# Performance work log

Measured on AMD Instinct MI355X. Metric: run time of the kernel, lower is better.

The kernel has to match this reference:

```python
import jax, jax.numpy as jnp
import numpy as np

N_NODES = 100000
N_EDGES = 1250000
F_RAW = 48      # raw node feature dim
F_LOC = 16      # location embedding dim
F1 = 48         # filters_1
F_OUT = 64      # out_channels


def _glorot(key, shape):
    fan_in, fan_out = shape[0], shape[1]
    scale = jnp.sqrt(6.0 / (fan_in + fan_out)).astype(jnp.float32)
    return jax.random.uniform(key, shape, jnp.float32, -1.0, 1.0) * scale


def setup_inputs() -> dict:
    key = jax.random.key(0)
    k_e, k_x, k_l, k_w1, k_w2 = jax.random.split(key, 5)
    edge_indices = jax.random.randint(k_e, (2, N_EDGES), 0, N_NODES, dtype=jnp.int64)
    features = jax.random.normal(k_x, (N_NODES, F_RAW), jnp.float32)
    location_embedding = jax.random.normal(k_l, (N_NODES, F_LOC), jnp.float32)
    W1 = _glorot(k_w1, (F_RAW + F_LOC, F1))
    b1 = jnp.zeros((F1,), jnp.float32)
    W2 = _glorot(k_w2, (F1 + F_LOC, F_OUT))
    b2 = jnp.zeros((F_OUT,), jnp.float32)
    return {"edge_indices": edge_indices, "features": features,
            "location_embedding": location_embedding,
            "W1": W1, "b1": b1, "W2": W2, "b2": b2}


def gcn_conv(x, src, dst, W, b, n_nodes):
    """PyG GCNConv: add self-loops, symmetric normalization, linear + bias."""
    h = x @ W  # [N, F_out]
    # degree counts include the self-loop (+1)
    deg = jnp.zeros((n_nodes,), h.dtype).at[dst].add(1.0) + 1.0
    dinv = jax.lax.rsqrt(deg)  # deg >= 1 so always finite
    coef = dinv[src] * dinv[dst]  # [E]
    agg = jnp.zeros((n_nodes, h.shape[1]), h.dtype).at[dst].add(h[src] * coef[:, None])
    # self-loop contribution: dinv[i]^2 * h[i]
    return agg + h * (dinv * dinv)[:, None] + b


def reference(edge_indices, features, location_embedding, W1, b1, W2, b2):
    src, dst = edge_indices[0], edge_indices[1]
    n = features.shape[0]
    x = jnp.concatenate([features, location_embedding], axis=-1)
    x = gcn_conv(x, src, dst, W1, b1, n)
    x = jax.nn.relu(x)
    # dropout is identity in eval mode (reference is inference semantics)
    x = jnp.concatenate([x, location_embedding], axis=-1)
    x = gcn_conv(x, src, dst, W2, b2, n)
    return x
```

## Files before the change

kernel.cpp:

```cpp
#include <hip/hip_runtime.h>
#include <hip/hip_fp16.h>

#define N_NODES 100000
#define N_EDGES 1250000
#define F_RAW 48
#define F_LOC 16
#define F1 48
#define F_OUT 64

#define NBUK 391
#define PADB 4096
#define NB2 500
#define CH2 (N_EDGES / NB2)

typedef _Float16 half8_t __attribute__((ext_vector_type(8)));
typedef float floatx4 __attribute__((ext_vector_type(4)));

__device__ void wprep_dev(const float* W, __half* Wpk, int M, int CT) {
    int lane = threadIdx.x;
    if (lane >= 64) return;
    for (int ct = 0; ct < CT; ++ct)
        for (int kt = 0; kt < 2; ++kt)
            for (int j = 0; j < 8; ++j) {
                int k = kt * 32 + (lane >> 4) * 8 + j;
                int c = ct * 16 + (lane & 15);
                Wpk[((ct * 2 + kt) * 64 + lane) * 8 + j] =
                    __float2half(W[k * M + c]);
            }
}

__device__ __forceinline__ void load_edge(const void* edges, int is32, int e,
                                          int& s, int& d) {
    if (is32) {
        const int* p = (const int*)edges;
        s = p[e];
        d = p[N_EDGES + e];
    } else {
        const long long* p = (const long long*)edges;
        s = (int)p[e];
        d = (int)p[N_EDGES + e];
    }
}

__global__ __launch_bounds__(512) void k_prep2(const void* edges,
                                               const float* W1, __half* wpk1,
                                               const float* W2, __half* wpk2,
                                               int* __restrict__ cursor,
                                               unsigned* __restrict__ binned) {
    int b = blockIdx.x, t = threadIdx.x;
    if (b >= NB2) {
        if (b == NB2)
            wprep_dev(W1, wpk1, F1, 3);
        else
            wprep_dev(W2, wpk2, F_OUT, 4);
        return;
    }
    __shared__ int hist[NBUK];
    __shared__ int2 stash[CH2];
    __shared__ int s_any;
    if (t == 0) s_any = 0;
    for (int k = t; k < NBUK; k += 512) hist[k] = 0;
    __syncthreads();
    int e0 = b * CH2;
    const unsigned* eu = (const unsigned*)edges;
    if (eu[2 * (e0 + t) + 1] != 0u) atomicOr(&s_any, 1);
    __syncthreads();
    int is32 = s_any;
    for (int i = t; i < CH2; i += 512) {
        int s, d;
        load_edge(edges, is32, e0 + i, s, d);
        int bk = d >> 8;
        stash[i] = make_int2(bk, ((d & 255) << 17) | s);
        atomicAdd(&hist[bk], 1);
    }
    __syncthreads();
    for (int k = t; k < NBUK; k += 512) {
        int c = hist[k];
        hist[k] = (c ? atomicAdd(&cursor[k], c) : 0) + k * PADB;
    }
    __syncthreads();
    for (int i = t; i < CH2; i += 512) {
        int2 sd = stash[i];
        int p = atomicAdd(&hist[sd.x], 1);
        binned[p] = (unsigned)sd.y;
    }
}

__global__ __launch_bounds__(256) void k_bucket(
    const unsigned* __restrict__ binned, const int* __restrict__ cursor,
    float* __restrict__ dinv, int2* __restrict__ rowse,
    unsigned* __restrict__ csr4) {
    int k = blockIdx.x, t = threadIdx.x;
    int lane = t & 63, wv = t >> 6;
    __shared__ int ldeg[256];
    __shared__ int wcnt[256];
    __shared__ int ws4[4];
    int base = k * PADB;
    int len = cursor[k];
    ldeg[t] = 0;
    __syncthreads();
    for (int i = t; i < len; i += 256)
        atomicAdd(&ldeg[binned[base + i] >> 17], 1);
    __syncthreads();
    int degv = ldeg[t];
    int x = degv;
#pragma unroll
    for (int off = 1; off < 64; off <<= 1) {
        int u = __shfl_up(x, off);
        if (lane >= off) x += u;
    }
    if (lane == 63) ws4[wv] = x;
    __syncthreads();
    int woff = 0;
    for (int w = 0; w < wv; ++w) woff += ws4[w];
    int excl = woff + x - degv;
    int node = k * 256 + t;
    if (node < N_NODES) {
        dinv[node] = rsqrtf((float)degv + 1.0f);
        rowse[node] = make_int2(base + excl, base + excl + degv);
    }
    wcnt[t] = base + excl;
    __syncthreads();
    for (int i = t; i < len; i += 256) {
        unsigned ent = binned[base + i];
        int p = atomicAdd(&wcnt[ent >> 17], 1);
        csr4[p] = ent & 0x1FFFFu;
    }
}

__global__ __launch_bounds__(256) void k_coef(unsigned* __restrict__ csr4,
                                              const float* __restrict__ dinv,
                                              const int* __restrict__ cursor) {
    int k = blockIdx.x;
    int end = k * PADB + cursor[k];
    for (int i = k * PADB + threadIdx.x; i < end; i += 256) {
        unsigned s = csr4[i];
        csr4[i] = (s << 14) | (unsigned)__half_as_ushort(__float2half(dinv[s]));
    }
}

__global__ __launch_bounds__(256) void k_gemm1(const float* __restrict__ feat,
                                               const float* __restrict__ loc,
                                               const __half* __restrict__ Wpk,
                                               __half* __restrict__ Y) {
    int wid = threadIdx.x >> 6;
    int lane = threadIdx.x & 63;
    int nb = (blockIdx.x * 4 + wid) * 32;
    if (nb >= N_NODES) return;
    half8_t b[3][2];
#pragma unroll
    for (int ct = 0; ct < 3; ++ct)
#pragma unroll
        for (int kt = 0; kt < 2; ++kt)
            b[ct][kt] = *reinterpret_cast<const half8_t*>(
                Wpk + ((ct * 2 + kt) * 64 + lane) * 8);
    int r = lane & 15;
    int slot = lane >> 4;
    half8_t a[2][2];
#pragma unroll
    for (int rt = 0; rt < 2; ++rt)
#pragma unroll
        for (int kt = 0; kt < 2; ++kt) {
            int sl = kt * 4 + slot;
            int node = nb + rt * 16 + r;
            const float* sp = (sl < 6)
                                  ? feat + (size_t)node * F_RAW + sl * 8
                                  : loc + (size_t)node * F_LOC + (sl - 6) * 8;
            float4 f0 = reinterpret_cast<const float4*>(sp)[0];
            float4 f1 = reinterpret_cast<const float4*>(sp)[1];
            half8_t h;
            h[0] = (_Float16)f0.x;
            h[1] = (_Float16)f0.y;
            h[2] = (_Float16)f0.z;
            h[3] = (_Float16)f0.w;
            h[4] = (_Float16)f1.x;
            h[5] = (_Float16)f1.y;
            h[6] = (_Float16)f1.z;
            h[7] = (_Float16)f1.w;
            a[rt][kt] = h;
        }
    floatx4 acc[2][3];
#pragma unroll
    for (int rt = 0; rt < 2; ++rt)
#pragma unroll
        for (int ct = 0; ct < 3; ++ct) {
            floatx4 z = {0.f, 0.f, 0.f, 0.f};
            z = __builtin_amdgcn_mfma_f32_16x16x32_f16(a[rt][0], b[ct][0], z, 0, 0, 0);
            z = __builtin_amdgcn_mfma_f32_16x16x32_f16(a[rt][1], b[ct][1], z, 0, 0, 0);
            acc[rt][ct] = z;
        }
    int row0 = (lane >> 4) * 4;
    int col = lane & 15;
#pragma unroll
    for (int rt = 0; rt < 2; ++rt)
#pragma unroll
        for (int ct = 0; ct < 3; ++ct)
#pragma unroll
            for (int j = 0; j < 4; ++j) {
                int node = nb + rt * 16 + row0 + j;
                Y[(size_t)node * 64 + ct * 16 + col] = __float2half(acc[rt][ct][j]);
            }
    int node = nb + (lane & 31);
    int slotp = 6 + (lane >> 5);
    *reinterpret_cast<int4*>(Y + (size_t)node * 64 + slotp * 8) =
        make_int4(0, 0, 0, 0);
}

__global__ __launch_bounds__(256) void k_gemm2(const __half* __restrict__ X,
                                               const __half* __restrict__ Wpk,
                                               __half* __restrict__ Y) {
    int wid = threadIdx.x >> 6;
    int lane = threadIdx.x & 63;
    int nb = (blockIdx.x * 4 + wid) * 32;
    if (nb >= N_NODES) return;
    half8_t b[4][2];
#pragma unroll
    for (int ct = 0; ct < 4; ++ct)
#pragma unroll
        for (int kt = 0; kt < 2; ++kt)
            b[ct][kt] = *reinterpret_cast<const half8_t*>(
                Wpk + ((ct * 2 + kt) * 64 + lane) * 8);
    int r = lane & 15;
    int ks = (lane >> 4) * 8;
    half8_t a[2][2];
#pragma unroll
    for (int rt = 0; rt < 2; ++rt)
#pragma unroll
        for (int kt = 0; kt < 2; ++kt)
            a[rt][kt] = *reinterpret_cast<const half8_t*>(
                X + ((size_t)(nb + rt * 16 + r) * 64 + kt * 32 + ks));
    floatx4 acc[2][4];
#pragma unroll
    for (int rt = 0; rt < 2; ++rt)
#pragma unroll
        for (int ct = 0; ct < 4; ++ct) {
            floatx4 z = {0.f, 0.f, 0.f, 0.f};
            z = __builtin_amdgcn_mfma_f32_16x16x32_f16(a[rt][0], b[ct][0], z, 0, 0, 0);
            z = __builtin_amdgcn_mfma_f32_16x16x32_f16(a[rt][1], b[ct][1], z, 0, 0, 0);
            acc[rt][ct] = z;
        }
    int row0 = (lane >> 4) * 4;
    int col = lane & 15;
#pragma unroll
    for (int rt = 0; rt < 2; ++rt)
#pragma unroll
        for (int ct = 0; ct < 4; ++ct)
#pragma unroll
            for (int j = 0; j < 4; ++j) {
                int node = nb + rt * 16 + row0 + j;
                Y[(size_t)node * 64 + ct * 16 + col] = __float2half(acc[rt][ct][j]);
            }
}

__device__ __forceinline__ __half2 c2_from(unsigned A) {
    unsigned b = A & 0x3FFFu;
    unsigned p = b | (b << 16);
    return *reinterpret_cast<__half2*>(&p);
}

__device__ __forceinline__ void fma8h(const int4& p, __half2 c2, __half2 a[4]) {
    const __half2* h = reinterpret_cast<const __half2*>(&p);
#pragma unroll
    for (int j = 0; j < 4; ++j) a[j] = __hfma2(h[j], c2, a[j]);
}

__device__ __forceinline__ __half2 shfl_xor_h2(__half2 v, int m) {
    int i = *reinterpret_cast<int*>(&v);
    i = __shfl_xor(i, m);
    return *reinterpret_cast<__half2*>(&i);
}

__global__ __launch_bounds__(256) void k_agg1(
    const __half* __restrict__ h1h, const float* __restrict__ dinv,
    const int2* __restrict__ rowse, const unsigned* __restrict__ csr4,
    const float* __restrict__ loc, const float* __restrict__ b1,
    __half* __restrict__ x1h) {
    int wave = threadIdx.x >> 6;
    int lane = threadIdx.x & 63;
    int grp = lane >> 3;
    int l8 = lane & 7;
    int node = blockIdx.x * 4 + wave;
    if (node >= N_NODES) return;
    int2 se = rowse[node];
    int r0 = se.x, r1 = se.y;
    const char* h1l = reinterpret_cast<const char*>(h1h) + (l8 << 4);
    float di = dinv[node];
    int4 hs = *reinterpret_cast<const int4*>(h1l + ((size_t)node << 7));
    int len = r1 - r0;
    int L = (len + 7) >> 3;
    int gs = r0 + grp * L;
    int ge = gs + L;
    if (ge > r1) ge = r1;
    __half2 z2 = __float2half2_rn(0.f);
    __half2 a0[4] = {z2, z2, z2, z2};
    __half2 a1[4] = {z2, z2, z2, z2};
    int e = gs;
    for (; e + 1 < ge; e += 2) {
        unsigned A = csr4[e];
        unsigned B = csr4[e + 1];
        int4 vA = *reinterpret_cast<const int4*>(h1l + ((A >> 14) << 7));
        int4 vB = *reinterpret_cast<const int4*>(h1l + ((B >> 14) << 7));
        fma8h(vA, c2_from(A), a0);
        fma8h(vB, c2_from(B), a1);
    }
    if (e < ge) {
        unsigned A = csr4[e];
        int4 vA = *reinterpret_cast<const int4*>(h1l + ((A >> 14) << 7));
        fma8h(vA, c2_from(A), a0);
    }
#pragma unroll
    for (int j = 0; j < 4; ++j) a0[j] = __hadd2(a0[j], a1[j]);
#pragma unroll
    for (int j = 0; j < 4; ++j) {
        a0[j] = __hadd2(a0[j], shfl_xor_h2(a0[j], 8));
        a0[j] = __hadd2(a0[j], shfl_xor_h2(a0[j], 16));
        a0[j] = __hadd2(a0[j], shfl_xor_h2(a0[j], 32));
    }
    if (lane < 8) {
        __half2 q[4];
        if (l8 < 6) {
            float d2 = di * di;
            const float4* b1v = reinterpret_cast<const float4*>(b1);
            float4 bA = b1v[l8 * 2];
            float4 bB = b1v[l8 * 2 + 1];
            float bb[8] = {bA.x, bA.y, bA.z, bA.w, bB.x, bB.y, bB.z, bB.w};
            const __half2* hh = reinterpret_cast<const __half2*>(&hs);
            float o[8];
#pragma unroll
            for (int j = 0; j < 4; ++j) {
                float2 t = __half22float2(hh[j]);
                float2 ag = __half22float2(a0[j]);
                o[2 * j] = fmaxf(fmaf(ag.x, di, fmaf(t.x, d2, bb[2 * j])), 0.f);
                o[2 * j + 1] =
                    fmaxf(fmaf(ag.y, di, fmaf(t.y, d2, bb[2 * j + 1])), 0.f);
            }
#pragma unroll
            for (int j = 0; j < 4; ++j)
                q[j] = __halves2half2(__float2half(o[2 * j]),
                                      __float2half(o[2 * j + 1]));
        } else {
            const float* lp = loc + (size_t)node * F_LOC + (l8 - 6) * 8;
            float4 f0 = reinterpret_cast<const float4*>(lp)[0];
            float4 f1 = reinterpret_cast<const float4*>(lp)[1];
            q[0] = __halves2half2(__float2half(f0.x), __float2half(f0.y));
            q[1] = __halves2half2(__float2half(f0.z), __float2half(f0.w));
            q[2] = __halves2half2(__float2half(f1.x), __float2half(f1.y));
            q[3] = __halves2half2(__float2half(f1.z), __float2half(f1.w));
        }
        reinterpret_cast<int4*>(x1h)[(size_t)node * 8 + l8] =
            *reinterpret_cast<int4*>(q);
    }
}

__global__ __launch_bounds__(256) void k_out(
    const __half* __restrict__ h2h, const float* __restrict__ dinv,
    const int2* __restrict__ rowse, const unsigned* __restrict__ csr4,
    const float* __restrict__ b2, float* __restrict__ out) {
    int wave = threadIdx.x >> 6;
    int lane = threadIdx.x & 63;
    int grp = lane >> 3;
    int l8 = lane & 7;
    int node = blockIdx.x * 4 + wave;
    if (node >= N_NODES) return;
    int2 se = rowse[node];
    int r0 = se.x, r1 = se.y;
    const char* h2l = reinterpret_cast<const char*>(h2h) + (l8 << 4);
    float di = dinv[node];
    int4 hs = *reinterpret_cast<const int4*>(h2l + ((size_t)node << 7));
    int len = r1 - r0;
    int L = (len + 7) >> 3;
    int gs = r0 + grp * L;
    int ge = gs + L;
    if (ge > r1) ge = r1;
    __half2 z2 = __float2half2_rn(0.f);
    __half2 a0[4] = {z2, z2, z2, z2};
    __half2 a1[4] = {z2, z2, z2, z2};
    int e = gs;
    for (; e + 1 < ge; e += 2) {
        unsigned A = csr4[e];
        unsigned B = csr4[e + 1];
        int4 vA = *reinterpret_cast<const int4*>(h2l + ((A >> 14) << 7));
        int4 vB = *reinterpret_cast<const int4*>(h2l + ((B >> 14) << 7));
        fma8h(vA, c2_from(A), a0);
        fma8h(vB, c2_from(B), a1);
    }
    if (e < ge) {
        unsigned A = csr4[e];
        int4 vA = *reinterpret_cast<const int4*>(h2l + ((A >> 14) << 7));
        fma8h(vA, c2_from(A), a0);
    }
#pragma unroll
    for (int j = 0; j < 4; ++j) a0[j] = __hadd2(a0[j], a1[j]);
#pragma unroll
    for (int j = 0; j < 4; ++j) {
        a0[j] = __hadd2(a0[j], shfl_xor_h2(a0[j], 8));
        a0[j] = __hadd2(a0[j], shfl_xor_h2(a0[j], 16));
        a0[j] = __hadd2(a0[j], shfl_xor_h2(a0[j], 32));
    }
    if (lane < 8) {
        float d2 = di * di;
        const float4* b2v = reinterpret_cast<const float4*>(b2);
        float4 bA = b2v[l8 * 2];
        float4 bB = b2v[l8 * 2 + 1];
        float bb[8] = {bA.x, bA.y, bA.z, bA.w, bB.x, bB.y, bB.z, bB.w};
        const __half2* hh = reinterpret_cast<const __half2*>(&hs);
        float o[8];
#pragma unroll
        for (int j = 0; j < 4; ++j) {
            float2 t = __half22float2(hh[j]);
            float2 ag = __half22float2(a0[j]);
            o[2 * j] = fmaf(ag.x, di, fmaf(t.x, d2, bb[2 * j]));
            o[2 * j + 1] = fmaf(ag.y, di, fmaf(t.y, d2, bb[2 * j + 1]));
        }
        float4* ov = reinterpret_cast<float4*>(out + (size_t)node * F_OUT);
        ov[l8 * 2] = make_float4(o[0], o[1], o[2], o[3]);
        ov[l8 * 2 + 1] = make_float4(o[4], o[5], o[6], o[7]);
    }
}

extern "C" void kernel_launch(void* const* d_in, const int* in_sizes, int n_in,
                              void* d_out, int out_size, void* d_ws,
                              size_t ws_size, hipStream_t stream) {
    const void* edges = d_in[0];
    const float* feat = (const float*)d_in[1];
    const float* loc = (const float*)d_in[2];
    const float* W1 = (const float*)d_in[3];
    const float* b1 = (const float*)d_in[4];
    const float* W2 = (const float*)d_in[5];
    const float* b2 = (const float*)d_in[6];
    float* out = (float*)d_out;

    char* ws = (char*)d_ws;
    float* dinv = (float*)(ws + 0);
    int2* rowse = (int2*)(ws + 400000);
    int* cursor = (int*)(ws + 1200000);
    unsigned* binned = (unsigned*)(ws + 1201664);
    unsigned* csr4 = (unsigned*)(ws + 7607808);
    __half* h1h = (__half*)(ws + 14013952);
    __half* x1h = (__half*)(ws + 26813952);
    __half* h2h = (__half*)(ws + 39613952);
    __half* wpk1 = (__half*)(ws + 52413952);
    __half* wpk2 = (__half*)(ws + 52420096);

    hipMemsetAsync(cursor, 0, NBUK * 4, stream);

    k_prep2<<<NB2 + 2, 512, 0, stream>>>(edges, W1, wpk1, W2, wpk2, cursor,
                                         binned);
    k_bucket<<<NBUK, 256, 0, stream>>>(binned, cursor, dinv, rowse, csr4);
    k_coef<<<NBUK, 256, 0, stream>>>(csr4, dinv, cursor);

    int gblocks = (N_NODES / 32 + 3) / 4;
    k_gemm1<<<gblocks, 256, 0, stream>>>(feat, loc, wpk1, h1h);
    k_agg1<<<(N_NODES + 3) / 4, 256, 0, stream>>>(h1h, dinv, rowse, csr4, loc,
                                                  b1, x1h);
    k_gemm2<<<gblocks, 256, 0, stream>>>(x1h, wpk2, h2h);
    k_out<<<(N_NODES + 3) / 4, 256, 0, stream>>>(h2h, dinv, rowse, csr4, b2,
                                                 out);
}
```

Before: 149.9 us.

## Fuse coef with gemm1 and fuse layer-1 aggregation with gemm2 via LDS

Merges the coefficient-packing kernel and the first GEMM into one launch, with block ranges split by blockIdx. Fuses the layer-1 aggregation with the second GEMM: each 512-thread block aggregates 32 nodes into an LDS tile, then runs MFMA on it to produce h2 directly. This removes the x1h global round-trip and two kernel launches. In exchange, each block now does both the gather-bound aggregation and the GEMM, and every wave waits at the sync for the slowest node in its tile.

```diff
diff --git a/kernel.cpp b/kernel.cpp
--- a/kernel.cpp
+++ b/kernel.cpp
@@ -12,6 +12,9 @@
 #define PADB 4096
 #define NB2 500
 #define CH2 (N_EDGES / NB2)
+
+#define GB1 ((N_NODES / 32 + 3) / 4)
+#define LROW 144
 
 typedef _Float16 half8_t __attribute__((ext_vector_type(8)));
 typedef float floatx4 __attribute__((ext_vector_type(4)));
@@ -128,24 +131,24 @@
     }
 }
 
-__global__ __launch_bounds__(256) void k_coef(unsigned* __restrict__ csr4,
-                                              const float* __restrict__ dinv,
-                                              const int* __restrict__ cursor) {
-    int k = blockIdx.x;
-    int end = k * PADB + cursor[k];
-    for (int i = k * PADB + threadIdx.x; i < end; i += 256) {
-        unsigned s = csr4[i];
-        csr4[i] = (s << 14) | (unsigned)__half_as_ushort(__float2half(dinv[s]));
-    }
-}
-
-__global__ __launch_bounds__(256) void k_gemm1(const float* __restrict__ feat,
-                                               const float* __restrict__ loc,
-                                               const __half* __restrict__ Wpk,
-                                               __half* __restrict__ Y) {
+__global__ __launch_bounds__(256) void k_cg1(
+    unsigned* __restrict__ csr4, const float* __restrict__ dinv,
+    const int* __restrict__ cursor, const float* __restrict__ feat,
+    const float* __restrict__ loc, const __half* __restrict__ Wpk,
+    __half* __restrict__ Y) {
+    if (blockIdx.x < NBUK) {
+        int k = blockIdx.x;
+        int end = k * PADB + cursor[k];
+        for (int i = k * PADB + threadIdx.x; i < end; i += 256) {
+            unsigned s = csr4[i];
+            csr4[i] =
+                (s << 14) | (unsigned)__half_as_ushort(__float2half(dinv[s]));
+        }
+        return;
+    }
     int wid = threadIdx.x >> 6;
     int lane = threadIdx.x & 63;
-    int nb = (blockIdx.x * 4 + wid) * 32;
+    int nb = ((blockIdx.x - NBUK) * 4 + wid) * 32;
     if (nb >= N_NODES) return;
     half8_t b[3][2];
 #pragma unroll
@@ -206,52 +209,6 @@
         make_int4(0, 0, 0, 0);
 }
 
-__global__ __launch_bounds__(256) void k_gemm2(const __half* __restrict__ X,
-                                               const __half* __restrict__ Wpk,
-                                               __half* __restrict__ Y) {
-    int wid = threadIdx.x >> 6;
-    int lane = threadIdx.x & 63;
-    int nb = (blockIdx.x * 4 + wid) * 32;
-    if (nb >= N_NODES) return;
-    half8_t b[4][2];
-#pragma unroll
-    for (int ct = 0; ct < 4; ++ct)
-#pragma unroll
-        for (int kt = 0; kt < 2; ++kt)
-            b[ct][kt] = *reinterpret_cast<const half8_t*>(
-                Wpk + ((ct * 2 + kt) * 64 + lane) * 8);
-    int r = lane & 15;
-    int ks = (lane >> 4) * 8;
-    half8_t a[2][2];
-#pragma unroll
-    for (int rt = 0; rt < 2; ++rt)
-#pragma unroll
-        for (int kt = 0; kt < 2; ++kt)
-            a[rt][kt] = *reinterpret_cast<const half8_t*>(
-                X + ((size_t)(nb + rt * 16 + r) * 64 + kt * 32 + ks));
-    floatx4 acc[2][4];
-#pragma unroll
-    for (int rt = 0; rt < 2; ++rt)
-#pragma unroll
-        for (int ct = 0; ct < 4; ++ct) {
-            floatx4 z = {0.f, 0.f, 0.f, 0.f};
-            z = __builtin_amdgcn_mfma_f32_16x16x32_f16(a[rt][0], b[ct][0], z, 0, 0, 0);
-            z = __builtin_amdgcn_mfma_f32_16x16x32_f16(a[rt][1], b[ct][1], z, 0, 0, 0);
-            acc[rt][ct] = z;
-        }
-    int row0 = (lane >> 4) * 4;
-    int col = lane & 15;
-#pragma unroll
-    for (int rt = 0; rt < 2; ++rt)
-#pragma unroll
-        for (int ct = 0; ct < 4; ++ct)
-#pragma unroll
-            for (int j = 0; j < 4; ++j) {
-                int node = nb + rt * 16 + row0 + j;
-                Y[(size_t)node * 64 + ct * 16 + col] = __float2half(acc[rt][ct][j]);
-            }
-}
-
 __device__ __forceinline__ __half2 c2_from(unsigned A) {
     unsigned b = A & 0x3FFFu;
     unsigned p = b | (b << 16);
@@ -270,85 +227,113 @@
     return *reinterpret_cast<__half2*>(&i);
 }
 
-__global__ __launch_bounds__(256) void k_agg1(
+__global__ __launch_bounds__(512) void k_aggemm(
     const __half* __restrict__ h1h, const float* __restrict__ dinv,
     const int2* __restrict__ rowse, const unsigned* __restrict__ csr4,
     const float* __restrict__ loc, const float* __restrict__ b1,
-    __half* __restrict__ x1h) {
-    int wave = threadIdx.x >> 6;
-    int lane = threadIdx.x & 63;
+    const __half* __restrict__ Wpk2, __half* __restrict__ h2h) {
+    __shared__ __align__(16) char lds_x1[32 * LROW];
+    int t = threadIdx.x;
+    int w = t >> 6;
+    int lane = t & 63;
     int grp = lane >> 3;
     int l8 = lane & 7;
-    int node = blockIdx.x * 4 + wave;
-    if (node >= N_NODES) return;
-    int2 se = rowse[node];
-    int r0 = se.x, r1 = se.y;
+    int nb = blockIdx.x * 32;
     const char* h1l = reinterpret_cast<const char*>(h1h) + (l8 << 4);
-    float di = dinv[node];
-    int4 hs = *reinterpret_cast<const int4*>(h1l + ((size_t)node << 7));
-    int len = r1 - r0;
-    int L = (len + 7) >> 3;
-    int gs = r0 + grp * L;
-    int ge = gs + L;
-    if (ge > r1) ge = r1;
-    __half2 z2 = __float2half2_rn(0.f);
-    __half2 a0[4] = {z2, z2, z2, z2};
-    __half2 a1[4] = {z2, z2, z2, z2};
-    int e = gs;
-    for (; e + 1 < ge; e += 2) {
-        unsigned A = csr4[e];
-        unsigned B = csr4[e + 1];
-        int4 vA = *reinterpret_cast<const int4*>(h1l + ((A >> 14) << 7));
-        int4 vB = *reinterpret_cast<const int4*>(h1l + ((B >> 14) << 7));
-        fma8h(vA, c2_from(A), a0);
-        fma8h(vB, c2_from(B), a1);
-    }
-    if (e < ge) {
-        unsigned A = csr4[e];
-        int4 vA = *reinterpret_cast<const int4*>(h1l + ((A >> 14) << 7));
-        fma8h(vA, c2_from(A), a0);
-    }
-#pragma unroll
-    for (int j = 0; j < 4; ++j) a0[j] = __hadd2(a0[j], a1[j]);
+#pragma unroll
+    for (int it = 0; it < 4; ++it) {
+        int nl = w * 4 + it;
+        int node = nb + nl;
+        int2 se = rowse[node];
+        int r0 = se.x, r1 = se.y;
+        float di = dinv[node];
+        int4 hs = *reinterpret_cast<const int4*>(h1l + ((size_t)node << 7));
+        int len = r1 - r0;
+        int L = (len + 7) >> 3;
+        int gs = r0 + grp * L;
+        int ge = gs + L;
+        if (ge > r1) ge = r1;
+        __half2 z2 = __float2half2_rn(0.f);
+        __half2 a0[4] = {z2, z2, z2, z2};
+        __half2 a1[4] = {z2, z2, z2, z2};
+        int e = gs;
+        for (; e + 1 < ge; e += 2) {
+            unsigned A = csr4[e];
+            unsigned B = csr4[e + 1];
+            int4 vA = *reinterpret_cast<const int4*>(h1l + ((A >> 14) << 7));
+            int4 vB = *reinterpret_cast<const int4*>(h1l + ((B >> 14) << 7));
+            fma8h(vA, c2_from(A), a0);
+            fma8h(vB, c2_from(B), a1);
+        }
+        if (e < ge) {
+            unsigned A = csr4[e];
+            int4 vA = *reinterpret_cast<const int4*>(h1l + ((A >> 14) << 7));
+            fma8h(vA, c2_from(A), a0);
+        }
+#pragma unroll
+        for (int j = 0; j < 4; ++j) a0[j] = __hadd2(a0[j], a1[j]);
+#pragma unroll
+        for (int j = 0; j < 4; ++j) {
+            a0[j] = __hadd2(a0[j], shfl_xor_h2(a0[j], 8));
+            a0[j] = __hadd2(a0[j], shfl_xor_h2(a0[j], 16));
+            a0[j] = __hadd2(a0[j], shfl_xor_h2(a0[j], 32));
+        }
+        if (lane < 8) {
+            __half2 q[4];
+            if (l8 < 6) {
+                float d2 = di * di;
+                const float4* b1v = reinterpret_cast<const float4*>(b1);
+                float4 bA = b1v[l8 * 2];
+                float4 bB = b1v[l8 * 2 + 1];
+                float bb[8] = {bA.x, bA.y, bA.z, bA.w, bB.x, bB.y, bB.z, bB.w};
+                const __half2* hh = reinterpret_cast<const __half2*>(&hs);
+#pragma unroll
+                for (int j = 0; j < 4; ++j) {
+                    float2 tt = __half22float2(hh[j]);
+                    float2 ag = __half22float2(a0[j]);
+                    float o0 =
+                        fmaxf(fmaf(ag.x, di, fmaf(tt.x, d2, bb[2 * j])), 0.f);
+                    float o1 = fmaxf(
+                        fmaf(ag.y, di, fmaf(tt.y, d2, bb[2 * j + 1])), 0.f);
+                    q[j] = __halves2half2(__float2half(o0), __float2half(o1));
+                }
+            } else {
+                const float* lp = loc + (size_t)node * F_LOC + (l8 - 6) * 8;
+                float4 f0 = reinterpret_cast<const float4*>(lp)[0];
+                float4 f1 = reinterpret_cast<const float4*>(lp)[1];
+                q[0] = __halves2half2(__float2half(f0.x), __float2half(f0.y));
+                q[1] = __halves2half2(__float2half(f0.z), __float2half(f0.w));
+                q[2] = __halves2half2(__float2half(f1.x), __float2half(f1.y));
+                q[3] = __halves2half2(__float2half(f1.z), __float2half(f1.w));
+            }
+            *reinterpret_cast<int4*>(&lds_x1[nl * LROW + l8 * 16]) =
+                *reinterpret_cast<int4*>(q);
+        }
+    }
+    __syncthreads();
+    int rt = w >> 2;
+    int ct = w & 3;
+    half8_t bfr[2];
+#pragma unroll
+    for (int kt = 0; kt < 2; ++kt)
+        bfr[kt] = *reinterpret_cast<const half8_t*>(
+            Wpk2 + ((ct * 2 + kt) * 64 + lane) * 8);
+    int r = lane & 15;
+    int ks = (lane >> 4) * 8;
+    half8_t afr[2];
+#pragma unroll
+    for (int kt = 0; kt < 2; ++kt)
+        afr[kt] = *reinterpret_cast<const half8_t*>(
+            &lds_x1[(rt * 16 + r) * LROW + kt * 64 + ks * 2]);
+    floatx4 z = {0.f, 0.f, 0.f, 0.f};
+    z = __builtin_amdgcn_mfma_f32_16x16x32_f16(afr[0], bfr[0], z, 0, 0, 0);
+    z = __builtin_amdgcn_mfma_f32_16x16x32_f16(afr[1], bfr[1], z, 0, 0, 0);
+    int row0 = (lane >> 4) * 4;
+    int col = lane & 15;
 #pragma unroll
     for (int j = 0; j < 4; ++j) {
-        a0[j] = __hadd2(a0[j], shfl_xor_h2(a0[j], 8));
-        a0[j] = __hadd2(a0[j], shfl_xor_h2(a0[j], 16));
-        a0[j] = __hadd2(a0[j], shfl_xor_h2(a0[j], 32));
-    }
-    if (lane < 8) {
-        __half2 q[4];
-        if (l8 < 6) {
-            float d2 = di * di;
-            const float4* b1v = reinterpret_cast<const float4*>(b1);
-            float4 bA = b1v[l8 * 2];
-            float4 bB = b1v[l8 * 2 + 1];
-            float bb[8] = {bA.x, bA.y, bA.z, bA.w, bB.x, bB.y, bB.z, bB.w};
-            const __half2* hh = reinterpret_cast<const __half2*>(&hs);
-            float o[8];
-#pragma unroll
-            for (int j = 0; j < 4; ++j) {
-                float2 t = __half22float2(hh[j]);
-                float2 ag = __half22float2(a0[j]);
-                o[2 * j] = fmaxf(fmaf(ag.x, di, fmaf(t.x, d2, bb[2 * j])), 0.f);
-                o[2 * j + 1] =
-                    fmaxf(fmaf(ag.y, di, fmaf(t.y, d2, bb[2 * j + 1])), 0.f);
-            }
-#pragma unroll
-            for (int j = 0; j < 4; ++j)
-                q[j] = __halves2half2(__float2half(o[2 * j]),
-                                      __float2half(o[2 * j + 1]));
-        } else {
-            const float* lp = loc + (size_t)node * F_LOC + (l8 - 6) * 8;
-            float4 f0 = reinterpret_cast<const float4*>(lp)[0];
-            float4 f1 = reinterpret_cast<const float4*>(lp)[1];
-            q[0] = __halves2half2(__float2half(f0.x), __float2half(f0.y));
-            q[1] = __halves2half2(__float2half(f0.z), __float2half(f0.w));
-            q[2] = __halves2half2(__float2half(f1.x), __float2half(f1.y));
-            q[3] = __halves2half2(__float2half(f1.z), __float2half(f1.w));
-        }
-        reinterpret_cast<int4*>(x1h)[(size_t)node * 8 + l8] =
-            *reinterpret_cast<int4*>(q);
+        int node = nb + rt * 16 + row0 + j;
+        h2h[(size_t)node * 64 + ct * 16 + col] = __float2half(z[j]);
     }
 }
 
@@ -437,23 +422,22 @@
     unsigned* binned = (unsigned*)(ws + 1201664);
     unsigned* csr4 = (unsigned*)(ws + 7607808);
     __half* h1h = (__half*)(ws + 14013952);
-    __half* x1h = (__half*)(ws + 26813952);
-    __half* h2h = (__half*)(ws + 39613952);
-    __half* wpk1 = (__half*)(ws + 52413952);
-    __half* wpk2 = (__half*)(ws + 52420096);
+    __half* h2h = (__half*)(ws + 26813952);
+    __half* wpk1 = (__half*)(ws + 39613952);
+    __half* wpk2 = (__half*)(ws + 39620096);
 
     hipMemsetAsync(cursor, 0, NBUK * 4, stream);
 
     k_prep2<<<NB2 + 2, 512, 0, stream>>>(edges, W1, wpk1, W2, wpk2, cursor,
                                          binned);
     k_bucket<<<NBUK, 256, 0, stream>>>(binned, cursor, dinv, rowse, csr4);
-    k_coef<<<NBUK, 256, 0, stream>>>(csr4, dinv, cursor);
-
-    int gblocks = (N_NODES / 32 + 3) / 4;
-    k_gemm1<<<gblocks, 256, 0, stream>>>(feat, loc, wpk1, h1h);
-    k_agg1<<<(N_NODES + 3) / 4, 256, 0, stream>>>(h1h, dinv, rowse, csr4, loc,
-                                                  b1, x1h);
-    k_gemm2<<<gblocks, 256, 0, stream>>>(x1h, wpk2, h2h);
+
+    k_cg1<<<NBUK + GB1, 256, 0, stream>>>(csr4, dinv, cursor, feat, loc, wpk1,
+                                          h1h);
+
+    k_aggemm<<<N_NODES / 32, 512, 0, stream>>>(h1h, dinv, rowse, csr4, loc,
+                                               b1, wpk2, h2h);
+
     k_out<<<(N_NODES + 3) / 4, 256, 0, stream>>>(h2h, dinv, rowse, csr4, b2,
                                                  out);
 }
```

Measured after the change: 145.5 us. 2.9% less time.
